# Kernel optimization log

Hardware: AMD Instinct MI355X
Metric: run time of the kernel (lower is better)

## Reference

```python
import jax, jax.numpy as jnp
import numpy as np

# dims: heads, batch, seq (== maxSentenceSize), embed, key/query dim, value dim
H, B, S, E, DK, DV = 16, 4, 1024, 1024, 64, 64
SCALE = int(np.sqrt(DK))  # original uses int(np.sqrt(keySize)) == 8


def setup_inputs() -> dict:
    key = jax.random.key(0)
    k = jax.random.split(key, 5)
    embeddings = jax.random.normal(k[0], (B, S, E), jnp.float32)
    # original init: uniform(0, 1) weights
    Wq = jax.random.uniform(k[1], (H, E, DK), jnp.float32)
    Wk = jax.random.uniform(k[2], (H, E, DK), jnp.float32)
    # note: original valueWeights are also sized (E, keySize)
    Wv = jax.random.uniform(k[3], (H, E, DK), jnp.float32)
    Wo = jax.random.uniform(k[4], (H * DV, E), jnp.float32)
    return {"embeddings": embeddings, "Wq": Wq, "Wk": Wk, "Wv": Wv, "Wo": Wo}


def _causal_mask(s):
    # 0 on/below diagonal, -inf above (matches the torch list-comprehension mask)
    return jnp.where(jnp.tril(jnp.ones((s, s), bool)), 0.0, -jnp.inf).astype(jnp.float32)


def reference(embeddings, Wq, Wk, Wv, Wo):
    # per-head projections, all heads batched: [H,B,S,d]
    q = jnp.einsum('bse,hed->hbsd', embeddings, Wq)
    kk = jnp.einsum('bse,hed->hbsd', embeddings, Wk)
    v = jnp.einsum('bse,hed->hbsd', embeddings, Wv)
    # FAITHFUL to original: keys are RESHAPED (flat reinterpretation [S,DK]->[DK,S]
    # per (head,batch) slice), NOT transposed.
    kT = kk.reshape(H, B, DK, S)
    mask = _causal_mask(S)  # [S,S]
    # softmax((QK_reshaped + mask) / int(sqrt(keySize)))
    scores = (jnp.einsum('hbsd,hbdt->hbst', q, kT) + mask) / SCALE
    attn = jax.nn.softmax(scores, axis=-1)  # [H,B,S,S]
    av = jnp.einsum('hbst,hbtd->hbsd', attn, v)  # [H,B,S,DV]
    # FAITHFUL to original: flat reshape [H,B,S,DV] -> [B,S,DV*H]
    concat = av.reshape(B, S, DV * H)
    return concat @ Wo  # [B,S,E]
```

## Files before the change

### kernel.cpp

```cpp
#include <hip/hip_runtime.h>
#include <math.h>

#define H 16
#define B 4
#define S 1024
#define E 1024
#define DK 64

typedef _Float16 f16x8 __attribute__((ext_vector_type(8)));
typedef _Float16 f16x4 __attribute__((ext_vector_type(4)));
typedef float    f32x4 __attribute__((ext_vector_type(4)));

__device__ __forceinline__ int swzb(int row, int colByte) {
    return row * 128 + (colByte ^ ((row & 7) << 4));
}

__global__ __launch_bounds__(256) void cvt_split_emb(const float* __restrict__ in,
                                                     _Float16* __restrict__ outH,
                                                     _Float16* __restrict__ outL) {
    int i = (blockIdx.x * 256 + threadIdx.x) * 8;
    float4 a = *(const float4*)&in[i];
    float4 b = *(const float4*)&in[i + 4];
    float x[8] = {a.x, a.y, a.z, a.w, b.x, b.y, b.z, b.w};
    f16x8 h, l;
    #pragma unroll
    for (int j = 0; j < 8; ++j) {
        _Float16 hh = (_Float16)x[j];
        h[j] = hh;
        l[j] = (_Float16)(x[j] - (float)hh);
    }
    *(f16x8*)&outH[i] = h;
    *(f16x8*)&outL[i] = l;
}

__global__ __launch_bounds__(256) void cvt_weights(
    const float* __restrict__ Wq, const float* __restrict__ Wk,
    const float* __restrict__ Wv, const float* __restrict__ Wo,
    _Float16* __restrict__ WTh, _Float16* __restrict__ WTl,
    _Float16* __restrict__ WoT) {
    __shared__ _Float16 Th[64 * 64];
    __shared__ _Float16 Tl[64 * 64];
    int tid = threadIdx.x;
    if (blockIdx.y < 48) {
        int et = blockIdx.x, chunk = blockIdx.y;
        const float* W = (chunk < 16 ? Wq : chunk < 32 ? Wk : Wv)
                         + (size_t)(chunk & 15) * E * DK;
        #pragma unroll
        for (int rr = 0; rr < 4; ++rr) {
            int u = rr * 256 + tid;
            int ei = u >> 4, f4 = u & 15;
            float4 v = *(const float4*)&W[(size_t)(et * 64 + ei) * 64 + f4 * 4];
            float x[4] = {v.x, v.y, v.z, v.w};
            f16x4 h, l;
            #pragma unroll
            for (int j = 0; j < 4; ++j) {
                _Float16 hh = (_Float16)x[j];
                h[j] = hh;
                l[j] = (_Float16)(x[j] - (float)hh);
            }
            *(f16x4*)((char*)Th + swzb(ei, f4 * 8)) = h;
            *(f16x4*)((char*)Tl + swzb(ei, f4 * 8)) = l;
        }
        __syncthreads();
        #pragma unroll
        for (int rr = 0; rr < 2; ++rr) {
            int u = rr * 256 + tid;
            int d = u >> 3, e8 = u & 7;
            f16x8 oh, ol;
            #pragma unroll
            for (int j = 0; j < 8; ++j) {
                int ei = e8 * 8 + j;
                oh[j] = *(_Float16*)((char*)Th + swzb(ei, d * 2));
                ol[j] = *(_Float16*)((char*)Tl + swzb(ei, d * 2));
            }
            size_t idx = (size_t)(chunk * 64 + d) * 1024 + et * 64 + e8 * 8;
            *(f16x8*)&WTh[idx] = oh;
            if (chunk < 32) *(f16x8*)&WTl[idx] = ol;
        }
    } else {
        int kt = blockIdx.x, nt = blockIdx.y - 48;
        #pragma unroll
        for (int rr = 0; rr < 4; ++rr) {
            int u = rr * 256 + tid;
            int ki = u >> 4, f4 = u & 15;
            float4 v = *(const float4*)&Wo[(size_t)(kt * 64 + ki) * 1024 + nt * 64 + f4 * 4];
            f16x4 o = { (_Float16)v.x, (_Float16)v.y, (_Float16)v.z, (_Float16)v.w };
            *(f16x4*)((char*)Th + swzb(ki, f4 * 8)) = o;
        }
        __syncthreads();
        #pragma unroll
        for (int rr = 0; rr < 2; ++rr) {
            int u = rr * 256 + tid;
            int nl = u >> 3, k8 = u & 7;
            f16x8 o;
            #pragma unroll
            for (int j = 0; j < 8; ++j) {
                int ki = k8 * 8 + j;
                o[j] = *(_Float16*)((char*)Th + swzb(ki, nl * 2));
            }
            *(f16x8*)&WoT[(size_t)(nt * 64 + nl) * 1024 + kt * 64 + k8 * 8] = o;
        }
    }
}

__global__ __launch_bounds__(256) void gemm_qkv(
    const _Float16* __restrict__ AH, const _Float16* __restrict__ AL,
    const _Float16* __restrict__ BTh, const _Float16* __restrict__ BTl,
    _Float16* __restrict__ QbH, _Float16* __restrict__ QbL,
    _Float16* __restrict__ kkTH, _Float16* __restrict__ kkTL,
    _Float16* __restrict__ V2) {
    __shared__ _Float16 SA[128 * 64];
    __shared__ _Float16 SB[128 * 64];
    int wg = ((int)blockIdx.x & 7) * 96 + ((int)blockIdx.x >> 3);
    int mt = wg / 24, nt = wg % 24;
    int r0 = mt * 128;
    int tid = threadIdx.x, lane = tid & 63, w = tid >> 6;
    int wr = w >> 1, wc = w & 1;
    int l15 = lane & 15, l4 = lane >> 4;

    f32x4 zero = {0.f, 0.f, 0.f, 0.f};
    f32x4 acc[4][4];
    #pragma unroll
    for (int i = 0; i < 4; ++i)
        #pragma unroll
        for (int j = 0; j < 4; ++j) acc[i][j] = zero;

    if (nt < 16) {
        int c0 = nt * 128;
        for (int kt = 0; kt < 32; ++kt) {
            __syncthreads();
            #pragma unroll
            for (int rr = 0; rr < 4; ++rr) {
                int u = rr * 256 + tid;
                int row = u >> 3, slot = u & 7;
                int c = slot ^ (row & 7);
                size_t kofs = (size_t)1024 * row + kt * 32 + (c & 3) * 8;
                const _Float16* sa = (c < 4 ? AH : AL) + (size_t)r0 * 1024 + kofs;
                const _Float16* sb = (c < 4 ? BTh : BTl) + (size_t)c0 * 1024 + kofs;
                __builtin_amdgcn_global_load_lds(sa, &SA[u * 8], 16, 0, 0);
                __builtin_amdgcn_global_load_lds(sb, &SB[u * 8], 16, 0, 0);
            }
            __syncthreads();

            f16x8 afH[4], afL[4], bfH[4], bfL[4];
            #pragma unroll
            for (int f = 0; f < 4; ++f) {
                int ar = wr * 64 + f * 16 + l15;
                int br = wc * 64 + f * 16 + l15;
                afH[f] = *(const f16x8*)((char*)SA + ar * 128 + ((l4    ) ^ (ar & 7)) * 16);
                afL[f] = *(const f16x8*)((char*)SA + ar * 128 + ((l4 + 4) ^ (ar & 7)) * 16);
                bfH[f] = *(const f16x8*)((char*)SB + br * 128 + ((l4    ) ^ (br & 7)) * 16);
                bfL[f] = *(const f16x8*)((char*)SB + br * 128 + ((l4 + 4) ^ (br & 7)) * 16);
            }
            #pragma unroll
            for (int i = 0; i < 4; ++i)
                #pragma unroll
                for (int j = 0; j < 4; ++j) {
                    acc[i][j] = __builtin_amdgcn_mfma_f32_16x16x32_f16(
                        afH[i], bfH[j], acc[i][j], 0, 0, 0);
                    acc[i][j] = __builtin_amdgcn_mfma_f32_16x16x32_f16(
                        afH[i], bfL[j], acc[i][j], 0, 0, 0);
                    acc[i][j] = __builtin_amdgcn_mfma_f32_16x16x32_f16(
                        afL[i], bfH[j], acc[i][j], 0, 0, 0);
                }
        }

        #pragma unroll
        for (int i = 0; i < 4; ++i) {
            int grow0 = r0 + wr * 64 + i * 16 + l4 * 4;
            #pragma unroll
            for (int j = 0; j < 4; ++j) {
                int gcol = c0 + wc * 64 + j * 16 + l15;
                if (gcol < 1024) {
                    int hh = gcol >> 6, dk = gcol & 63;
                    #pragma unroll
                    for (int r = 0; r < 4; ++r) {
                        int grow = grow0 + r;
                        int bb = grow >> 10, s = grow & 1023;
                        float v = acc[i][j][r];
                        _Float16 h = (_Float16)v;
                        size_t idx = (((size_t)hh * 4 + bb) * 1024 + s) * 64 + dk;
                        QbH[idx] = h;
                        QbL[idx] = (_Float16)(v - (float)h);
                    }
                } else {
                    int hh = (gcol >> 6) & 15, dk = gcol & 63;
                    #pragma unroll
                    for (int r = 0; r < 4; ++r) {
                        int grow = grow0 + r;
                        int bb = grow >> 10, s = grow & 1023;
                        float v = acc[i][j][r];
                        _Float16 h = (_Float16)v;
                        size_t idx = (((size_t)hh * 4 + bb) * 64 + (s >> 4)) * 1024
                                     + (s & 15) * 64 + dk;
                        kkTH[idx] = h;
                        kkTL[idx] = (_Float16)(v - (float)h);
                    }
                }
            }
        }
    } else {
        int c0 = 2048 + (nt - 16) * 128;
        for (int kt = 0; kt < 16; ++kt) {
            __syncthreads();
            #pragma unroll
            for (int rr = 0; rr < 4; ++rr) {
                int u = rr * 256 + tid;
                int row = u >> 3, slot = u & 7;
                int c = slot ^ (row & 7);
                size_t ga = (size_t)(r0 + row) * 1024 + kt * 64 + c * 8;
                size_t gb = (size_t)(c0 + row) * 1024 + kt * 64 + c * 8;
                __builtin_amdgcn_global_load_lds(&AH[ga],  &SA[u * 8], 16, 0, 0);
                __builtin_amdgcn_global_load_lds(&BTh[gb], &SB[u * 8], 16, 0, 0);
            }
            __syncthreads();

            #pragma unroll
            for (int ks = 0; ks < 2; ++ks) {
                f16x8 af[4], bf[4];
                #pragma unroll
                for (int f = 0; f < 4; ++f) {
                    int ar = wr * 64 + f * 16 + l15;
                    int br = wc * 64 + f * 16 + l15;
                    af[f] = *(const f16x8*)((char*)SA + ar * 128 + ((ks * 4 + l4) ^ (ar & 7)) * 16);
                    bf[f] = *(const f16x8*)((char*)SB + br * 128 + ((ks * 4 + l4) ^ (br & 7)) * 16);
                }
                #pragma unroll
                for (int i = 0; i < 4; ++i)
                    #pragma unroll
                    for (int j = 0; j < 4; ++j)
                        acc[i][j] = __builtin_amdgcn_mfma_f32_16x16x32_f16(
                            af[i], bf[j], acc[i][j], 0, 0, 0);
            }
        }

        #pragma unroll
        for (int i = 0; i < 4; ++i) {
            int grow0 = r0 + wr * 64 + i * 16 + l4 * 4;
            int bb = grow0 >> 10, s = grow0 & 1023;
            #pragma unroll
            for (int j = 0; j < 4; ++j) {
                int gcol = c0 + wc * 64 + j * 16 + l15;
                int hh = (gcol >> 6) & 15, dv = gcol & 63;
                f16x4 o = { (_Float16)acc[i][j][0], (_Float16)acc[i][j][1],
                            (_Float16)acc[i][j][2], (_Float16)acc[i][j][3] };
                *(f16x4*)&V2[(((size_t)hh * 4 + bb) * 64 + dv) * 1024 + s] = o;
            }
        }
    }
}

__global__ __launch_bounds__(256) void trans_k(const _Float16* __restrict__ kkTH,
                                               const _Float16* __restrict__ kkTL,
                                               _Float16* __restrict__ K2H,
                                               _Float16* __restrict__ K2L) {
    int tt = blockIdx.x;
    size_t hb = blockIdx.y;
    int mode = blockIdx.z;
    const _Float16* src = mode ? kkTL : kkTH;
    _Float16* dst = mode ? K2L : K2H;
    __shared__ _Float16 T[64 * 64];
    int tid = threadIdx.x;
    #pragma unroll
    for (int rr = 0; rr < 2; ++rr) {
        int u = rr * 256 + tid;
        int d = u >> 3, c8 = u & 7;
        f16x8 v = *(const f16x8*)&src[(hb * 64 + d) * 1024 + tt * 64 + c8 * 8];
        *(f16x8*)((char*)T + swzb(d, c8 * 16)) = v;
    }
    __syncthreads();
    #pragma unroll
    for (int rr = 0; rr < 2; ++rr) {
        int u = rr * 256 + tid;
        int ti = u >> 3, d8 = u & 7;
        f16x8 o;
        #pragma unroll
        for (int j = 0; j < 8; ++j)
            o[j] = *(_Float16*)((char*)T + swzb(d8 * 8 + j, ti * 2));
        *(f16x8*)&dst[(hb * 1024 + tt * 64 + ti) * 64 + d8 * 8] = o;
    }
}

__global__ __launch_bounds__(256) void attn(
    const _Float16* __restrict__ QbH, const _Float16* __restrict__ QbL,
    const _Float16* __restrict__ K2H, const _Float16* __restrict__ K2L,
    const _Float16* __restrict__ V2, _Float16* __restrict__ CC) {
    int qt = 15 - (int)blockIdx.x;
    int b = blockIdx.y, h = blockIdx.z;
    size_t hb = (size_t)h * 4 + b;
    __shared__ _Float16 QsH[64 * 64], QsL[64 * 64];
    __shared__ _Float16 KsH[64 * 64], KsL[64 * 64];
    __shared__ _Float16 Vs[64 * 64], Ps[64 * 64];
    int tid = threadIdx.x, lane = tid & 63, w = tid >> 6;
    int l15 = lane & 15, l4 = lane >> 4;
    int s0 = qt * 64;

    #pragma unroll
    for (int rr = 0; rr < 2; ++rr) {
        int u = rr * 256 + tid, row = u >> 3, c8 = u & 7;
        size_t gi = (hb * 1024 + s0 + row) * 64 + c8 * 8;
        int off = swzb(row, c8 * 16);
        *(f16x8*)((char*)QsH + off) = *(const f16x8*)&QbH[gi];
        *(f16x8*)((char*)QsL + off) = *(const f16x8*)&QbL[gi];
    }
    f16x8 rkH[2], rkL[2], rv[2];
    #pragma unroll
    for (int rr = 0; rr < 2; ++rr) {
        int u = rr * 256 + tid, row = u >> 3, c8 = u & 7;
        size_t ki = (hb * 1024 + row) * 64 + c8 * 8;
        rkH[rr] = *(const f16x8*)&K2H[ki];
        rkL[rr] = *(const f16x8*)&K2L[ki];
        rv[rr]  = *(const f16x8*)&V2[(hb * 64 + row) * 1024 + c8 * 8];
    }
    __syncthreads();
    int srow = w * 16 + l15;
    f16x8 qfH[2], qfL[2];
    #pragma unroll
    for (int ks = 0; ks < 2; ++ks) {
        int kb = (ks * 32 + l4 * 8) * 2;
        qfH[ks] = *(const f16x8*)((char*)QsH + swzb(srow, kb));
        qfL[ks] = *(const f16x8*)((char*)QsL + swzb(srow, kb));
    }

    float m = -__builtin_inff(), lsum = 0.f;
    f32x4 zero = {0.f, 0.f, 0.f, 0.f};
    f32x4 acc2[4] = {zero, zero, zero, zero};
    int sg = s0 + srow;
    int ntile = qt + 1;

    for (int tt = 0; tt < ntile; ++tt) {
        int t0 = tt * 64;
        __syncthreads();
        #pragma unroll
        for (int rr = 0; rr < 2; ++rr) {
            int u = rr * 256 + tid, row = u >> 3, c8 = u & 7;
            int off = swzb(row, c8 * 16);
            *(f16x8*)((char*)KsH + off) = rkH[rr];
            *(f16x8*)((char*)KsL + off) = rkL[rr];
            *(f16x8*)((char*)Vs + off)  = rv[rr];
        }
        if (tt + 1 < ntile) {
            int t0n = t0 + 64;
            #pragma unroll
            for (int rr = 0; rr < 2; ++rr) {
                int u = rr * 256 + tid, row = u >> 3, c8 = u & 7;
                size_t ki = (hb * 1024 + t0n + row) * 64 + c8 * 8;
                rkH[rr] = *(const f16x8*)&K2H[ki];
                rkL[rr] = *(const f16x8*)&K2L[ki];
                rv[rr]  = *(const f16x8*)&V2[(hb * 64 + row) * 1024 + t0n + c8 * 8];
            }
        }
        __syncthreads();

        f32x4 z[4] = {zero, zero, zero, zero};
        __builtin_amdgcn_s_setprio(1);
        #pragma unroll
        for (int ks = 0; ks < 2; ++ks) {
            int kb = (ks * 32 + l4 * 8) * 2;
            #pragma unroll
            for (int f = 0; f < 4; ++f) {
                int trow = f * 16 + l15;
                f16x8 akH = *(const f16x8*)((char*)KsH + swzb(trow, kb));
                f16x8 akL = *(const f16x8*)((char*)KsL + swzb(trow, kb));
                z[f] = __builtin_amdgcn_mfma_f32_16x16x32_f16(akH, qfH[ks], z[f], 0, 0, 0);
                z[f] = __builtin_amdgcn_mfma_f32_16x16x32_f16(akH, qfL[ks], z[f], 0, 0, 0);
                z[f] = __builtin_amdgcn_mfma_f32_16x16x32_f16(akL, qfH[ks], z[f], 0, 0, 0);
            }
        }
        __builtin_amdgcn_s_setprio(0);
        float mt = -__builtin_inff();
        #pragma unroll
        for (int f = 0; f < 4; ++f)
            #pragma unroll
            for (int r = 0; r < 4; ++r) {
                int tg = t0 + f * 16 + l4 * 4 + r;
                float val = z[f][r] * 0.125f;
                val = (tg > sg) ? -__builtin_inff() : val;
                z[f][r] = val;
                mt = fmaxf(mt, val);
            }
        mt = fmaxf(mt, __shfl_xor(mt, 16));
        mt = fmaxf(mt, __shfl_xor(mt, 32));
        float mn = fmaxf(m, mt);
        float corr = __expf(m - mn);
        float ps = 0.f;
        #pragma unroll
        for (int f = 0; f < 4; ++f)
            #pragma unroll
            for (int r = 0; r < 4; ++r) {
                float p = __expf(z[f][r] - mn);
                z[f][r] = p;
                ps += p;
            }
        ps += __shfl_xor(ps, 16);
        ps += __shfl_xor(ps, 32);
        lsum = lsum * corr + ps;
        m = mn;
        #pragma unroll
        for (int f = 0; f < 4; ++f) acc2[f] *= corr;

        #pragma unroll
        for (int f = 0; f < 4; ++f) {
            f16x4 pk = { (_Float16)z[f][0], (_Float16)z[f][1],
                         (_Float16)z[f][2], (_Float16)z[f][3] };
            *(f16x4*)((char*)Ps + swzb(srow, (f * 16 + l4 * 4) * 2)) = pk;
        }
        __builtin_amdgcn_s_setprio(1);
        #pragma unroll
        for (int ks = 0; ks < 2; ++ks) {
            int kb = (ks * 32 + l4 * 8) * 2;
            f16x8 bp = *(const f16x8*)((char*)Ps + swzb(srow, kb));
            #pragma unroll
            for (int f = 0; f < 4; ++f) {
                int dvrow = f * 16 + l15;
                f16x8 av = *(const f16x8*)((char*)Vs + swzb(dvrow, kb));
                acc2[f] = __builtin_amdgcn_mfma_f32_16x16x32_f16(av, bp, acc2[f], 0, 0, 0);
            }
        }
        __builtin_amdgcn_s_setprio(0);
    }

    float inv = 1.f / lsum;
    int sp = s0 + srow;
    int bprow = h >> 2;
    int spp = (h & 3) * 256 + b * 64 + (sp >> 4);
    int cb = (sp & 15) * 64;
    #pragma unroll
    for (int f = 0; f < 4; ++f) {
        int dv = f * 16 + l4 * 4;
        f16x4 o = { (_Float16)(acc2[f][0] * inv), (_Float16)(acc2[f][1] * inv),
                    (_Float16)(acc2[f][2] * inv), (_Float16)(acc2[f][3] * inv) };
        *(f16x4*)&CC[((size_t)bprow * 1024 + spp) * 1024 + cb + dv] = o;
    }
}

__global__ __launch_bounds__(256) void gemm_out(
    const _Float16* __restrict__ A, const _Float16* __restrict__ BT,
    float* __restrict__ out) {
    __shared__ _Float16 As[128 * 64];
    __shared__ _Float16 Bs[128 * 64];
    int wg = ((int)blockIdx.x & 7) * 32 + ((int)blockIdx.x >> 3);
    int mt = wg >> 3, nt = wg & 7;
    int r0 = mt * 128, c0 = nt * 128;
    int tid = threadIdx.x, lane = tid & 63, w = tid >> 6;
    int wr = w >> 1, wc = w & 1;
    int l15 = lane & 15, l4 = lane >> 4;

    f32x4 zero = {0.f, 0.f, 0.f, 0.f};
    f32x4 acc[4][4];
    #pragma unroll
    for (int i = 0; i < 4; ++i)
        #pragma unroll
        for (int j = 0; j < 4; ++j) acc[i][j] = zero;

    for (int kt = 0; kt < 16; ++kt) {
        __syncthreads();
        #pragma unroll
        for (int rr = 0; rr < 4; ++rr) {
            int u = rr * 256 + tid;
            int row = u >> 3, slot = u & 7;
            int c = slot ^ (row & 7);
            size_t ga = (size_t)(r0 + row) * 1024 + kt * 64 + c * 8;
            size_t gb = (size_t)(c0 + row) * 1024 + kt * 64 + c * 8;
            __builtin_amdgcn_global_load_lds(&A[ga],  &As[u * 8], 16, 0, 0);
            __builtin_amdgcn_global_load_lds(&BT[gb], &Bs[u * 8], 16, 0, 0);
        }
        __syncthreads();

        #pragma unroll
        for (int ks = 0; ks < 2; ++ks) {
            f16x8 af[4], bf[4];
            #pragma unroll
            for (int f = 0; f < 4; ++f) {
                int ar = wr * 64 + f * 16 + l15;
                int br = wc * 64 + f * 16 + l15;
                af[f] = *(const f16x8*)((char*)As + ar * 128 + ((ks * 4 + l4) ^ (ar & 7)) * 16);
                bf[f] = *(const f16x8*)((char*)Bs + br * 128 + ((ks * 4 + l4) ^ (br & 7)) * 16);
            }
            #pragma unroll
            for (int i = 0; i < 4; ++i)
                #pragma unroll
                for (int j = 0; j < 4; ++j)
                    acc[i][j] = __builtin_amdgcn_mfma_f32_16x16x32_f16(
                        af[i], bf[j], acc[i][j], 0, 0, 0);
        }
    }

    #pragma unroll
    for (int i = 0; i < 4; ++i) {
        int grow0 = r0 + wr * 64 + i * 16 + l4 * 4;
        #pragma unroll
        for (int j = 0; j < 4; ++j) {
            int gcol = c0 + wc * 64 + j * 16 + l15;
            #pragma unroll
            for (int r = 0; r < 4; ++r)
                out[(size_t)(grow0 + r) * 1024 + gcol] = acc[i][j][r];
        }
    }
}

extern "C" void kernel_launch(void* const* d_in, const int* in_sizes, int n_in,
                              void* d_out, int out_size, void* d_ws, size_t ws_size,
                              hipStream_t stream) {
    const float* emb = (const float*)d_in[0];
    const float* Wq  = (const float*)d_in[1];
    const float* Wk  = (const float*)d_in[2];
    const float* Wv  = (const float*)d_in[3];
    const float* Wo  = (const float*)d_in[4];
    float* out = (float*)d_out;

    _Float16* embH = (_Float16*)d_ws;
    _Float16* embL = embH + 4194304;
    _Float16* WTh  = embL + 4194304;
    _Float16* WTl  = WTh + 3145728;
    _Float16* WoT  = WTl + 2097152;
    _Float16* QbH  = WoT + 1048576;
    _Float16* QbL  = QbH + 4194304;
    _Float16* V2   = QbL + 4194304;
    _Float16* K2H  = embH;
    _Float16* K2L  = embL;
    _Float16* CC   = WTh;
    _Float16* kkTH = (_Float16*)d_out;
    _Float16* kkTL = kkTH + 4194304;

    cvt_split_emb<<<2048, 256, 0, stream>>>(emb, embH, embL);
    cvt_weights  <<<dim3(16, 64), 256, 0, stream>>>(Wq, Wk, Wv, Wo, WTh, WTl, WoT);
    gemm_qkv     <<<768, 256, 0, stream>>>(embH, embL, WTh, WTl,
                                           QbH, QbL, kkTH, kkTL, V2);
    trans_k      <<<dim3(16, 64, 2), 256, 0, stream>>>(kkTH, kkTL, K2H, K2L);
    attn         <<<dim3(16, 4, 16), 256, 0, stream>>>(QbH, QbL, K2H, K2L, V2, CC);
    gemm_out     <<<256, 256, 0, stream>>>(CC, WoT, out);
}
```

Baseline: 259.1 us.

## Merge prep kernels, drop LDS staging in attention, remove swizzles, XCD-aware mapping

Merges the embedding and weight conversion kernels into a single prep launch. The attention kernel now reads K, V and Q fragments straight from global memory instead of staging them in LDS, and it remaps blocks so each XCD handles a fixed set of head/batch pairs for L2 locality. The GEMMs drop the XOR swizzle on their LDS layouts, and gemm_qkv splits hi/lo planes into separate LDS regions. The risks are more LDS bank conflicts without the swizzle and higher global/L2 latency in the attention inner loop, since it no longer prefetches into shared memory.

```diff
diff --git a/kernel.cpp b/kernel.cpp
--- a/kernel.cpp
+++ b/kernel.cpp
@@ -15,36 +15,37 @@
     return row * 128 + (colByte ^ ((row & 7) << 4));
 }
 
-__global__ __launch_bounds__(256) void cvt_split_emb(const float* __restrict__ in,
-                                                     _Float16* __restrict__ outH,
-                                                     _Float16* __restrict__ outL) {
-    int i = (blockIdx.x * 256 + threadIdx.x) * 8;
-    float4 a = *(const float4*)&in[i];
-    float4 b = *(const float4*)&in[i + 4];
-    float x[8] = {a.x, a.y, a.z, a.w, b.x, b.y, b.z, b.w};
-    f16x8 h, l;
-    #pragma unroll
-    for (int j = 0; j < 8; ++j) {
-        _Float16 hh = (_Float16)x[j];
-        h[j] = hh;
-        l[j] = (_Float16)(x[j] - (float)hh);
-    }
-    *(f16x8*)&outH[i] = h;
-    *(f16x8*)&outL[i] = l;
-}
-
-__global__ __launch_bounds__(256) void cvt_weights(
+__global__ __launch_bounds__(256) void prep(
+    const float* __restrict__ emb,
     const float* __restrict__ Wq, const float* __restrict__ Wk,
     const float* __restrict__ Wv, const float* __restrict__ Wo,
+    _Float16* __restrict__ embH, _Float16* __restrict__ embL,
     _Float16* __restrict__ WTh, _Float16* __restrict__ WTl,
     _Float16* __restrict__ WoT) {
     __shared__ _Float16 Th[64 * 64];
     __shared__ _Float16 Tl[64 * 64];
-    int tid = threadIdx.x;
-    if (blockIdx.y < 48) {
-        int et = blockIdx.x, chunk = blockIdx.y;
-        const float* W = (chunk < 16 ? Wq : chunk < 32 ? Wk : Wv)
-                         + (size_t)(chunk & 15) * E * DK;
+    int bid = blockIdx.x, tid = threadIdx.x;
+    if (bid < 2048) {
+        int i = (bid * 256 + tid) * 8;
+        float4 a = *(const float4*)&emb[i];
+        float4 bb = *(const float4*)&emb[i + 4];
+        float x[8] = {a.x, a.y, a.z, a.w, bb.x, bb.y, bb.z, bb.w};
+        f16x8 hv, lv;
+        #pragma unroll
+        for (int j = 0; j < 8; ++j) {
+            _Float16 hh = (_Float16)x[j];
+            hv[j] = hh;
+            lv[j] = (_Float16)(x[j] - (float)hh);
+        }
+        *(f16x8*)&embH[i] = hv;
+        *(f16x8*)&embL[i] = lv;
+        return;
+    }
+    int idx = bid - 2048;
+    int et = idx & 15, cy = idx >> 4;
+    if (cy < 48) {
+        const float* W = (cy < 16 ? Wq : cy < 32 ? Wk : Wv)
+                         + (size_t)(cy & 15) * E * DK;
         #pragma unroll
         for (int rr = 0; rr < 4; ++rr) {
             int u = rr * 256 + tid;
@@ -73,12 +74,12 @@
                 oh[j] = *(_Float16*)((char*)Th + swzb(ei, d * 2));
                 ol[j] = *(_Float16*)((char*)Tl + swzb(ei, d * 2));
             }
-            size_t idx = (size_t)(chunk * 64 + d) * 1024 + et * 64 + e8 * 8;
-            *(f16x8*)&WTh[idx] = oh;
-            if (chunk < 32) *(f16x8*)&WTl[idx] = ol;
+            size_t o = (size_t)(cy * 64 + d) * 1024 + et * 64 + e8 * 8;
+            *(f16x8*)&WTh[o] = oh;
+            if (cy < 32) *(f16x8*)&WTl[o] = ol;
         }
     } else {
-        int kt = blockIdx.x, nt = blockIdx.y - 48;
+        int kt = et, nt = cy - 48;
         #pragma unroll
         for (int rr = 0; rr < 4; ++rr) {
             int u = rr * 256 + tid;
@@ -130,27 +131,28 @@
         for (int kt = 0; kt < 32; ++kt) {
             __syncthreads();
             #pragma unroll
-            for (int rr = 0; rr < 4; ++rr) {
+            for (int rr = 0; rr < 2; ++rr) {
                 int u = rr * 256 + tid;
-                int row = u >> 3, slot = u & 7;
-                int c = slot ^ (row & 7);
-                size_t kofs = (size_t)1024 * row + kt * 32 + (c & 3) * 8;
-                const _Float16* sa = (c < 4 ? AH : AL) + (size_t)r0 * 1024 + kofs;
-                const _Float16* sb = (c < 4 ? BTh : BTl) + (size_t)c0 * 1024 + kofs;
-                __builtin_amdgcn_global_load_lds(sa, &SA[u * 8], 16, 0, 0);
-                __builtin_amdgcn_global_load_lds(sb, &SB[u * 8], 16, 0, 0);
+                int row = u >> 2, c8 = u & 3;
+                size_t ga = (size_t)(r0 + row) * 1024 + kt * 32 + c8 * 8;
+                size_t gb = (size_t)(c0 + row) * 1024 + kt * 32 + c8 * 8;
+                __builtin_amdgcn_global_load_lds(&AH[ga],  &SA[u * 8], 16, 0, 0);
+                __builtin_amdgcn_global_load_lds(&AL[ga],  &SA[4096 + u * 8], 16, 0, 0);
+                __builtin_amdgcn_global_load_lds(&BTh[gb], &SB[u * 8], 16, 0, 0);
+                __builtin_amdgcn_global_load_lds(&BTl[gb], &SB[4096 + u * 8], 16, 0, 0);
             }
             __syncthreads();
 
+            int kb = l4 * 16;
             f16x8 afH[4], afL[4], bfH[4], bfL[4];
             #pragma unroll
             for (int f = 0; f < 4; ++f) {
                 int ar = wr * 64 + f * 16 + l15;
                 int br = wc * 64 + f * 16 + l15;
-                afH[f] = *(const f16x8*)((char*)SA + ar * 128 + ((l4    ) ^ (ar & 7)) * 16);
-                afL[f] = *(const f16x8*)((char*)SA + ar * 128 + ((l4 + 4) ^ (ar & 7)) * 16);
-                bfH[f] = *(const f16x8*)((char*)SB + br * 128 + ((l4    ) ^ (br & 7)) * 16);
-                bfL[f] = *(const f16x8*)((char*)SB + br * 128 + ((l4 + 4) ^ (br & 7)) * 16);
+                afH[f] = *(const f16x8*)((char*)SA + ar * 64 + kb);
+                afL[f] = *(const f16x8*)((char*)SA + 8192 + ar * 64 + kb);
+                bfH[f] = *(const f16x8*)((char*)SB + br * 64 + kb);
+                bfL[f] = *(const f16x8*)((char*)SB + 8192 + br * 64 + kb);
             }
             #pragma unroll
             for (int i = 0; i < 4; ++i)
@@ -178,10 +180,10 @@
                         int grow = grow0 + r;
                         int bb = grow >> 10, s = grow & 1023;
                         float v = acc[i][j][r];
-                        _Float16 h = (_Float16)v;
-                        size_t idx = (((size_t)hh * 4 + bb) * 1024 + s) * 64 + dk;
-                        QbH[idx] = h;
-                        QbL[idx] = (_Float16)(v - (float)h);
+                        _Float16 hq = (_Float16)v;
+                        size_t o = (((size_t)hh * 4 + bb) * 1024 + s) * 64 + dk;
+                        QbH[o] = hq;
+                        QbL[o] = (_Float16)(v - (float)hq);
                     }
                 } else {
                     int hh = (gcol >> 6) & 15, dk = gcol & 63;
@@ -190,26 +192,25 @@
                         int grow = grow0 + r;
                         int bb = grow >> 10, s = grow & 1023;
                         float v = acc[i][j][r];
-                        _Float16 h = (_Float16)v;
-                        size_t idx = (((size_t)hh * 4 + bb) * 64 + (s >> 4)) * 1024
-                                     + (s & 15) * 64 + dk;
-                        kkTH[idx] = h;
-                        kkTL[idx] = (_Float16)(v - (float)h);
+                        _Float16 hq = (_Float16)v;
+                        size_t o = (((size_t)hh * 4 + bb) * 64 + (s >> 4)) * 1024
+                                   + (s & 15) * 64 + dk;
+                        kkTH[o] = hq;
+                        kkTL[o] = (_Float16)(v - (float)hq);
                     }
                 }
             }
         }
     } else {
-        int c0 = 2048 + (nt - 16) * 128;
+        int c0 = (nt - 16) * 128;
         for (int kt = 0; kt < 16; ++kt) {
             __syncthreads();
             #pragma unroll
             for (int rr = 0; rr < 4; ++rr) {
                 int u = rr * 256 + tid;
-                int row = u >> 3, slot = u & 7;
-                int c = slot ^ (row & 7);
-                size_t ga = (size_t)(r0 + row) * 1024 + kt * 64 + c * 8;
-                size_t gb = (size_t)(c0 + row) * 1024 + kt * 64 + c * 8;
+                int row = u >> 3, c8 = u & 7;
+                size_t ga = (size_t)(r0 + row) * 1024 + kt * 64 + c8 * 8;
+                size_t gb = (size_t)(2048 + c0 + row) * 1024 + kt * 64 + c8 * 8;
                 __builtin_amdgcn_global_load_lds(&AH[ga],  &SA[u * 8], 16, 0, 0);
                 __builtin_amdgcn_global_load_lds(&BTh[gb], &SB[u * 8], 16, 0, 0);
             }
@@ -217,13 +218,14 @@
 
             #pragma unroll
             for (int ks = 0; ks < 2; ++ks) {
+                int kb = (ks * 32 + l4 * 8) * 2;
                 f16x8 af[4], bf[4];
                 #pragma unroll
                 for (int f = 0; f < 4; ++f) {
                     int ar = wr * 64 + f * 16 + l15;
                     int br = wc * 64 + f * 16 + l15;
-                    af[f] = *(const f16x8*)((char*)SA + ar * 128 + ((ks * 4 + l4) ^ (ar & 7)) * 16);
-                    bf[f] = *(const f16x8*)((char*)SB + br * 128 + ((ks * 4 + l4) ^ (br & 7)) * 16);
+                    af[f] = *(const f16x8*)((char*)SA + ar * 128 + kb);
+                    bf[f] = *(const f16x8*)((char*)SB + br * 128 + kb);
                 }
                 #pragma unroll
                 for (int i = 0; i < 4; ++i)
@@ -241,7 +243,7 @@
             #pragma unroll
             for (int j = 0; j < 4; ++j) {
                 int gcol = c0 + wc * 64 + j * 16 + l15;
-                int hh = (gcol >> 6) & 15, dv = gcol & 63;
+                int hh = gcol >> 6, dv = gcol & 63;
                 f16x4 o = { (_Float16)acc[i][j][0], (_Float16)acc[i][j][1],
                             (_Float16)acc[i][j][2], (_Float16)acc[i][j][3] };
                 *(f16x4*)&V2[(((size_t)hh * 4 + bb) * 64 + dv) * 1024 + s] = o;
@@ -285,83 +287,44 @@
     const _Float16* __restrict__ QbH, const _Float16* __restrict__ QbL,
     const _Float16* __restrict__ K2H, const _Float16* __restrict__ K2L,
     const _Float16* __restrict__ V2, _Float16* __restrict__ CC) {
-    int qt = 15 - (int)blockIdx.x;
-    int b = blockIdx.y, h = blockIdx.z;
-    size_t hb = (size_t)h * 4 + b;
-    __shared__ _Float16 QsH[64 * 64], QsL[64 * 64];
-    __shared__ _Float16 KsH[64 * 64], KsL[64 * 64];
-    __shared__ _Float16 Vs[64 * 64], Ps[64 * 64];
+    int bid = blockIdx.x;
+    int xcd = bid & 7, slot = bid >> 3;
+    int hbi = xcd * 8 + (slot >> 4);
+    int qt = 15 - (slot & 15);
+    int h = hbi >> 2, b = hbi & 3;
+    size_t hb = (size_t)hbi;
+    __shared__ _Float16 Ps[64 * 64];
     int tid = threadIdx.x, lane = tid & 63, w = tid >> 6;
     int l15 = lane & 15, l4 = lane >> 4;
     int s0 = qt * 64;
-
-    #pragma unroll
-    for (int rr = 0; rr < 2; ++rr) {
-        int u = rr * 256 + tid, row = u >> 3, c8 = u & 7;
-        size_t gi = (hb * 1024 + s0 + row) * 64 + c8 * 8;
-        int off = swzb(row, c8 * 16);
-        *(f16x8*)((char*)QsH + off) = *(const f16x8*)&QbH[gi];
-        *(f16x8*)((char*)QsL + off) = *(const f16x8*)&QbL[gi];
-    }
-    f16x8 rkH[2], rkL[2], rv[2];
-    #pragma unroll
-    for (int rr = 0; rr < 2; ++rr) {
-        int u = rr * 256 + tid, row = u >> 3, c8 = u & 7;
-        size_t ki = (hb * 1024 + row) * 64 + c8 * 8;
-        rkH[rr] = *(const f16x8*)&K2H[ki];
-        rkL[rr] = *(const f16x8*)&K2L[ki];
-        rv[rr]  = *(const f16x8*)&V2[(hb * 64 + row) * 1024 + c8 * 8];
-    }
-    __syncthreads();
     int srow = w * 16 + l15;
+    int sg = s0 + srow;
+
     f16x8 qfH[2], qfL[2];
     #pragma unroll
     for (int ks = 0; ks < 2; ++ks) {
-        int kb = (ks * 32 + l4 * 8) * 2;
-        qfH[ks] = *(const f16x8*)((char*)QsH + swzb(srow, kb));
-        qfL[ks] = *(const f16x8*)((char*)QsL + swzb(srow, kb));
+        size_t qa = (hb * 1024 + s0 + srow) * 64 + ks * 32 + l4 * 8;
+        qfH[ks] = *(const f16x8*)&QbH[qa];
+        qfL[ks] = *(const f16x8*)&QbL[qa];
     }
 
     float m = -__builtin_inff(), lsum = 0.f;
     f32x4 zero = {0.f, 0.f, 0.f, 0.f};
     f32x4 acc2[4] = {zero, zero, zero, zero};
-    int sg = s0 + srow;
     int ntile = qt + 1;
 
     for (int tt = 0; tt < ntile; ++tt) {
         int t0 = tt * 64;
-        __syncthreads();
-        #pragma unroll
-        for (int rr = 0; rr < 2; ++rr) {
-            int u = rr * 256 + tid, row = u >> 3, c8 = u & 7;
-            int off = swzb(row, c8 * 16);
-            *(f16x8*)((char*)KsH + off) = rkH[rr];
-            *(f16x8*)((char*)KsL + off) = rkL[rr];
-            *(f16x8*)((char*)Vs + off)  = rv[rr];
-        }
-        if (tt + 1 < ntile) {
-            int t0n = t0 + 64;
-            #pragma unroll
-            for (int rr = 0; rr < 2; ++rr) {
-                int u = rr * 256 + tid, row = u >> 3, c8 = u & 7;
-                size_t ki = (hb * 1024 + t0n + row) * 64 + c8 * 8;
-                rkH[rr] = *(const f16x8*)&K2H[ki];
-                rkL[rr] = *(const f16x8*)&K2L[ki];
-                rv[rr]  = *(const f16x8*)&V2[(hb * 64 + row) * 1024 + t0n + c8 * 8];
-            }
-        }
-        __syncthreads();
-
         f32x4 z[4] = {zero, zero, zero, zero};
         __builtin_amdgcn_s_setprio(1);
         #pragma unroll
         for (int ks = 0; ks < 2; ++ks) {
-            int kb = (ks * 32 + l4 * 8) * 2;
             #pragma unroll
             for (int f = 0; f < 4; ++f) {
                 int trow = f * 16 + l15;
-                f16x8 akH = *(const f16x8*)((char*)KsH + swzb(trow, kb));
-                f16x8 akL = *(const f16x8*)((char*)KsL + swzb(trow, kb));
+                size_t ka = (hb * 1024 + t0 + trow) * 64 + ks * 32 + l4 * 8;
+                f16x8 akH = *(const f16x8*)&K2H[ka];
+                f16x8 akL = *(const f16x8*)&K2L[ka];
                 z[f] = __builtin_amdgcn_mfma_f32_16x16x32_f16(akH, qfH[ks], z[f], 0, 0, 0);
                 z[f] = __builtin_amdgcn_mfma_f32_16x16x32_f16(akH, qfL[ks], z[f], 0, 0, 0);
                 z[f] = __builtin_amdgcn_mfma_f32_16x16x32_f16(akL, qfH[ks], z[f], 0, 0, 0);
@@ -413,7 +376,8 @@
             #pragma unroll
             for (int f = 0; f < 4; ++f) {
                 int dvrow = f * 16 + l15;
-                f16x8 av = *(const f16x8*)((char*)Vs + swzb(dvrow, kb));
+                size_t va = (hb * 64 + dvrow) * 1024 + t0 + ks * 32 + l4 * 8;
+                f16x8 av = *(const f16x8*)&V2[va];
                 acc2[f] = __builtin_amdgcn_mfma_f32_16x16x32_f16(av, bp, acc2[f], 0, 0, 0);
             }
         }
@@ -458,10 +422,9 @@
         #pragma unroll
         for (int rr = 0; rr < 4; ++rr) {
             int u = rr * 256 + tid;
-            int row = u >> 3, slot = u & 7;
-            int c = slot ^ (row & 7);
-            size_t ga = (size_t)(r0 + row) * 1024 + kt * 64 + c * 8;
-            size_t gb = (size_t)(c0 + row) * 1024 + kt * 64 + c * 8;
+            int row = u >> 3, c8 = u & 7;
+            size_t ga = (size_t)(r0 + row) * 1024 + kt * 64 + c8 * 8;
+            size_t gb = (size_t)(c0 + row) * 1024 + kt * 64 + c8 * 8;
             __builtin_amdgcn_global_load_lds(&A[ga],  &As[u * 8], 16, 0, 0);
             __builtin_amdgcn_global_load_lds(&BT[gb], &Bs[u * 8], 16, 0, 0);
         }
@@ -469,13 +432,14 @@
 
         #pragma unroll
         for (int ks = 0; ks < 2; ++ks) {
+            int kb = (ks * 32 + l4 * 8) * 2;
             f16x8 af[4], bf[4];
             #pragma unroll
             for (int f = 0; f < 4; ++f) {
                 int ar = wr * 64 + f * 16 + l15;
                 int br = wc * 64 + f * 16 + l15;
-                af[f] = *(const f16x8*)((char*)As + ar * 128 + ((ks * 4 + l4) ^ (ar & 7)) * 16);
-                bf[f] = *(const f16x8*)((char*)Bs + br * 128 + ((ks * 4 + l4) ^ (br & 7)) * 16);
+                af[f] = *(const f16x8*)((char*)As + ar * 128 + kb);
+                bf[f] = *(const f16x8*)((char*)Bs + br * 128 + kb);
             }
             #pragma unroll
             for (int i = 0; i < 4; ++i)
@@ -523,11 +487,11 @@
     _Float16* kkTH = (_Float16*)d_out;
     _Float16* kkTL = kkTH + 4194304;
 
-    cvt_split_emb<<<2048, 256, 0, stream>>>(emb, embH, embL);
-    cvt_weights  <<<dim3(16, 64), 256, 0, stream>>>(Wq, Wk, Wv, Wo, WTh, WTl, WoT);
-    gemm_qkv     <<<768, 256, 0, stream>>>(embH, embL, WTh, WTl,
-                                           QbH, QbL, kkTH, kkTL, V2);
-    trans_k      <<<dim3(16, 64, 2), 256, 0, stream>>>(kkTH, kkTL, K2H, K2L);
-    attn         <<<dim3(16, 4, 16), 256, 0, stream>>>(QbH, QbL, K2H, K2L, V2, CC);
-    gemm_out     <<<256, 256, 0, stream>>>(CC, WoT, out);
-}
+    prep     <<<3072, 256, 0, stream>>>(emb, Wq, Wk, Wv, Wo,
+                                        embH, embL, WTh, WTl, WoT);
+    gemm_qkv <<<768, 256, 0, stream>>>(embH, embL, WTh, WTl,
+                                       QbH, QbL, kkTH, kkTL, V2);
+    trans_k  <<<dim3(16, 64, 2), 256, 0, stream>>>(kkTH, kkTL, K2H, K2L);
+    attn     <<<1024, 256, 0, stream>>>(QbH, QbL, K2H, K2L, V2, CC);
+    gemm_out <<<256, 256, 0, stream>>>(CC, WoT, out);
+}
```

After: 373.9 us. 44.3% more time.
